# Optimization experiments

Measured on AMD Instinct MI355X. Metric: run time of the kernel, lower is better.

Reference implementation:

```python
import jax, jax.numpy as jnp
import numpy as np

N, E, ET, C, H, L = 100000, 500000, 3, 128, 128, 3
LN_EPS = 1e-5
L2_EPS = 1e-12


def setup_inputs() -> dict:
    ks = jax.random.split(jax.random.key(0), 12)
    s = 0.05
    return {
        "x": jax.random.normal(ks[0], (N, C), jnp.float32),
        "edges": jax.random.randint(ks[1], (ET, 2, E), 0, N),
        "Wp": jax.random.normal(ks[2], (ET, C, C), jnp.float32) * s,
        "bp": jax.random.normal(ks[3], (ET, C), jnp.float32) * s,
        "Wl0": jax.random.normal(ks[4], (ET, C, H), jnp.float32) * s,
        "bl0": jax.random.normal(ks[5], (ET, H), jnp.float32) * s,
        "Wr0": jax.random.normal(ks[6], (ET, C, H), jnp.float32) * s,
        "Wl": jax.random.normal(ks[7], (L - 1, ET, H, H), jnp.float32) * s,
        "bl": jax.random.normal(ks[8], (L - 1, ET, H), jnp.float32) * s,
        "Wr": jax.random.normal(ks[9], (L - 1, ET, H, H), jnp.float32) * s,
        "ln_g": jnp.ones((L - 1, H), jnp.float32),
        "ln_b": jnp.zeros((L - 1, H), jnp.float32),
    }


def _mean_aggr(msg, dst, n):
    # scatter-mean of per-edge messages onto destination nodes
    summed = jax.ops.segment_sum(msg, dst, num_segments=n)
    deg = jax.ops.segment_sum(jnp.ones((dst.shape[0],), msg.dtype), dst, num_segments=n)
    return summed / jnp.maximum(deg, 1.0)[:, None]


def _sage(h, ei, Wl_, bl_, Wr_, Wp_=None, bp_=None, normalize=False):
    # PyG SAGEConv: out = lin_l(mean_{j in N(i)} h_j) + lin_r(h_i)
    src, dst = ei[0], ei[1]
    hs = jax.nn.relu(h @ Wp_ + bp_) if Wp_ is not None else h  # project=True path
    agg = _mean_aggr(hs[src], dst, h.shape[0])
    out = agg @ Wl_ + bl_ + h @ Wr_
    if normalize:
        out = out / jnp.maximum(jnp.linalg.norm(out, axis=-1, keepdims=True), L2_EPS)
    return out


def _layer_norm(h, g, b):
    mu = h.mean(-1, keepdims=True)
    var = ((h - mu) ** 2).mean(-1, keepdims=True)
    return (h - mu) / jnp.sqrt(var + LN_EPS) * g + b


def _forward(x, edges, Wp, bp, Wl0, bl0, Wr0, Wl, bl, Wr, ln_g, ln_b):
    et = edges.shape[0]
    # layer 0: project=True, normalize=True; HeteroConv mean over edge types
    h = sum(_sage(x, edges[t], Wl0[t], bl0[t], Wr0[t], Wp[t], bp[t], True)
            for t in range(et)) / et
    h = _layer_norm(jax.nn.relu(h), ln_g[0], ln_b[0])  # dropout = identity (eval)
    n_rest = Wl.shape[0]
    for l in range(n_rest):
        h = sum(_sage(h, edges[t], Wl[l, t], bl[l, t], Wr[l, t])
                for t in range(et)) / et
        if l != n_rest - 1:
            h = _layer_norm(jax.nn.relu(h), ln_g[l + 1], ln_b[l + 1])
    return h


def reference(x, edges, Wp, bp, Wl0, bl0, Wr0, Wl, bl, Wr, ln_g, ln_b):
    return _forward(x, edges, Wp, bp, Wl0, bl0, Wr0, Wl, bl, Wr, ln_g, ln_b)
```

## Files before the change

### kernel.cpp

```cpp
#include <hip/hip_runtime.h>
#include <math.h>

#define CH 128
#define ETC 3
#define LN_EPS 1e-5f

typedef unsigned short u16;
typedef unsigned int u32;
typedef __attribute__((ext_vector_type(8))) short short8;
typedef __attribute__((ext_vector_type(4))) float f32x4;

__device__ __forceinline__ u16 f2bf(float f) {
    u32 u = __float_as_uint(f);
    u += 0x7FFFu + ((u >> 16) & 1u);
    return (u16)(u >> 16);
}
__device__ __forceinline__ float bflo(u32 u) { return __uint_as_float(u << 16); }
__device__ __forceinline__ float bfhi(u32 u) { return __uint_as_float(u & 0xFFFF0000u); }

__device__ __forceinline__ f32x4 mfma16(short8 a, short8 b, f32x4 c) {
    return __builtin_amdgcn_mfma_f32_16x16x32_bf16(a, b, c, 0, 0, 0);
}
__device__ __forceinline__ short8 ld8(const u16* p) { return *(const short8*)p; }

__global__ __launch_bounds__(256) void pack_w(
    const float* __restrict__ Wp, const float* __restrict__ Wl0,
    const float* __restrict__ Wr0, const float* __restrict__ Wl,
    const float* __restrict__ Wr, const float* __restrict__ bl,
    u16* __restrict__ Bswz, float* __restrict__ bls)
{
    if (blockIdx.x == 0) {
        int l = threadIdx.x >> 7, i = threadIdx.x & 127;
        bls[threadIdx.x] = (bl[((size_t)l * ETC + 0) * CH + i] +
                            bl[((size_t)l * ETC + 1) * CH + i] +
                            bl[((size_t)l * ETC + 2) * CH + i]) * (1.f / 3.f);
    }
    int grp = blockIdx.x * 256 + threadIdx.x;
    if (grp >= 17 * 2048) return;
    int lane = grp & 63;
    int t1 = grp >> 6;
    int nt = t1 & 7, t2 = t1 >> 3;
    int s = t2 & 3, mat = t2 >> 2;
    int q = lane >> 4, c = lane & 15;
    int nn = nt * 16 + c;

    const float* s0;
    const float* s1 = nullptr;
    const float* s2 = nullptr;
    float scale = 1.f;
    if (mat < 3) {
        s0 = Wp + (size_t)mat * CH * CH;
    } else if (mat < 9) {
        int t = (mat - 3) >> 1;
        s0 = ((mat - 3) & 1) ? Wr0 + (size_t)t * CH * CH : Wl0 + (size_t)t * CH * CH;
    } else {
        int l = (mat < 13) ? 0 : 1;
        int mm = mat - (l ? 13 : 9);
        scale = 1.f / 3.f;
        if (mm < 3) s0 = Wl + ((size_t)l * ETC + mm) * CH * CH;
        else {
            s0 = Wr + ((size_t)l * ETC + 0) * CH * CH;
            s1 = s0 + CH * CH;
            s2 = s1 + CH * CH;
        }
    }
    short8 o;
    #pragma unroll
    for (int j = 0; j < 8; ++j) {
        int k = s * 32 + q * 8 + j;
        float v = s0[(size_t)k * CH + nn];
        if (s1) v += s1[(size_t)k * CH + nn] + s2[(size_t)k * CH + nn];
        o[j] = (short)f2bf(v * scale);
    }
    *(short8*)&Bswz[(size_t)grp * 8] = o;
}

__global__ __launch_bounds__(256) void cast_x(
    const float* __restrict__ x, u16* __restrict__ xb, int total)
{
    int i = (blockIdx.x * 256 + threadIdx.x) * 8;
    if (i >= total) return;
    short8 o;
    #pragma unroll
    for (int j = 0; j < 8; ++j) o[j] = (short)f2bf(x[i + j]);
    *(short8*)&xb[i] = o;
}

template<int MODE, int RF>
__global__ __launch_bounds__(256, 2) void combine_k(
    const u16* __restrict__ agg0, const u16* __restrict__ agg1,
    const u16* __restrict__ agg2, const u16* __restrict__ self,
    const u16* __restrict__ Bs, const float* __restrict__ bias,
    const float* __restrict__ lg, const float* __restrict__ lb,
    u16* __restrict__ outb, float* __restrict__ outf, int nrows)
{
    __shared__ __align__(16) u16 Bsh[CH * CH];
    const int tid = threadIdx.x;
    const int w = tid >> 6, lane = tid & 63;
    const int q = lane >> 4, c = lane & 15;
    const int rbase = (blockIdx.x * 4 + w) * (RF * 16);
    const u16* aggs[3] = {agg0, agg1, agg2};
    constexpr int NM = (MODE == 0) ? 6 : ((MODE == 3) ? 1 : 4);

    f32x4 acc[RF][8] = {};
    f32x4 res[RF][8] = {};

    #pragma unroll
    for (int m = 0; m < NM; ++m) {
        __syncthreads();
        const u16* bsrc = Bs + (size_t)m * CH * CH;
        #pragma unroll
        for (int i = 0; i < 8; ++i)
            *(short8*)&Bsh[(i * 256 + tid) * 8] = ld8(&bsrc[(i * 256 + tid) * 8]);
        __syncthreads();

        const u16* A;
        if constexpr (MODE == 0)      A = (m & 1) ? self : aggs[m >> 1];
        else if constexpr (MODE == 3) A = self;
        else                          A = (m < 3) ? aggs[m] : self;

        #pragma unroll
        for (int s = 0; s < 4; ++s) {
            short8 af[RF];
            #pragma unroll
            for (int rf = 0; rf < RF; ++rf)
                af[rf] = ld8(&A[(size_t)(rbase + rf * 16 + c) * CH + s * 32 + q * 8]);
            #pragma unroll
            for (int nt = 0; nt < 8; ++nt) {
                short8 bv = *(const short8*)&Bsh[((size_t)(s * 8 + nt) * 64 + lane) * 8];
                #pragma unroll
                for (int rf = 0; rf < RF; ++rf)
                    acc[rf][nt] = mfma16(af[rf], bv, acc[rf][nt]);
            }
        }

        if constexpr (MODE == 0) {
            if (m & 1) {
                const int t = m >> 1;
                #pragma unroll
                for (int rf = 0; rf < RF; ++rf) {
                    float ss[4] = {0.f, 0.f, 0.f, 0.f};
                    #pragma unroll
                    for (int nt = 0; nt < 8; ++nt) {
                        float bf = bias[t * CH + nt * 16 + c];
                        #pragma unroll
                        for (int r = 0; r < 4; ++r) {
                            float v = acc[rf][nt][r] + bf;
                            acc[rf][nt][r] = v;
                            ss[r] += v * v;
                        }
                    }
                    #pragma unroll
                    for (int msk = 1; msk < 16; msk <<= 1)
                        #pragma unroll
                        for (int r = 0; r < 4; ++r) ss[r] += __shfl_xor(ss[r], msk, 64);
                    float sc[4];
                    #pragma unroll
                    for (int r = 0; r < 4; ++r)
                        sc[r] = 1.f / (3.f * fmaxf(sqrtf(ss[r]), 1e-12f));
                    #pragma unroll
                    for (int nt = 0; nt < 8; ++nt)
                        #pragma unroll
                        for (int r = 0; r < 4; ++r) {
                            res[rf][nt][r] += acc[rf][nt][r] * sc[r];
                            acc[rf][nt][r] = 0.f;
                        }
                }
            }
        }
    }

    if constexpr (MODE != 0) {
        #pragma unroll
        for (int nt = 0; nt < 8; ++nt) {
            float bv = bias[nt * 16 + c];
            #pragma unroll
            for (int rf = 0; rf < RF; ++rf)
                #pragma unroll
                for (int r = 0; r < 4; ++r) res[rf][nt][r] = acc[rf][nt][r] + bv;
        }
    }

    if constexpr (MODE == 2) {
        #pragma unroll
        for (int rf = 0; rf < RF; ++rf)
            #pragma unroll
            for (int nt = 0; nt < 8; ++nt)
                #pragma unroll
                for (int r = 0; r < 4; ++r) {
                    int row = rbase + rf * 16 + q * 4 + r;
                    if (row < nrows) outf[(size_t)row * CH + nt * 16 + c] = res[rf][nt][r];
                }
        return;
    }

    if constexpr (MODE == 3) {
        #pragma unroll
        for (int rf = 0; rf < RF; ++rf)
            #pragma unroll
            for (int nt = 0; nt < 8; ++nt)
                #pragma unroll
                for (int r = 0; r < 4; ++r) {
                    int row = rbase + rf * 16 + q * 4 + r;
                    outb[(size_t)row * CH + nt * 16 + c] = f2bf(fmaxf(res[rf][nt][r], 0.f));
                }
        return;
    }

    #pragma unroll
    for (int rf = 0; rf < RF; ++rf) {
        float s1[4] = {0.f, 0.f, 0.f, 0.f}, s2[4] = {0.f, 0.f, 0.f, 0.f};
        #pragma unroll
        for (int nt = 0; nt < 8; ++nt)
            #pragma unroll
            for (int r = 0; r < 4; ++r) {
                float v = fmaxf(res[rf][nt][r], 0.f);
                res[rf][nt][r] = v;
                s1[r] += v;
                s2[r] += v * v;
            }
        #pragma unroll
        for (int msk = 1; msk < 16; msk <<= 1)
            #pragma unroll
            for (int r = 0; r < 4; ++r) {
                s1[r] += __shfl_xor(s1[r], msk, 64);
                s2[r] += __shfl_xor(s2[r], msk, 64);
            }
        float mu[4], rs[4];
        #pragma unroll
        for (int r = 0; r < 4; ++r) {
            mu[r] = s1[r] * (1.f / 128.f);
            float var = s2[r] * (1.f / 128.f) - mu[r] * mu[r];
            rs[r] = rsqrtf(var + LN_EPS);
        }
        #pragma unroll
        for (int nt = 0; nt < 8; ++nt) {
            float gv = lg[nt * 16 + c], bv = lb[nt * 16 + c];
            #pragma unroll
            for (int r = 0; r < 4; ++r) {
                int row = rbase + rf * 16 + q * 4 + r;
                outb[(size_t)row * CH + nt * 16 + c] =
                    f2bf((res[rf][nt][r] - mu[r]) * rs[r] * gv + bv);
            }
        }
    }
}

__global__ __launch_bounds__(256) void agg_k(
    const u16* __restrict__ msg, const int* __restrict__ rowptr,
    const int* __restrict__ col, u16* __restrict__ agg, int n,
    int Ecap, unsigned long long aggstride)
{
    const int t = blockIdx.y;
    rowptr += (size_t)t * (n + 1);
    col += (size_t)t * Ecap;
    agg += (size_t)t * aggstride;

    int gid = blockIdx.x * 256 + threadIdx.x;
    int node = gid >> 5;
    int lane = threadIdx.x & 31;
    if (node >= n) return;
    int s = rowptr[node], e = rowptr[node + 1];
    const uint2* m64 = (const uint2*)msg;
    float a0 = 0.f, a1 = 0.f, a2 = 0.f, a3 = 0.f;
    float b0 = 0.f, b1 = 0.f, b2 = 0.f, b3 = 0.f;
    int j = s;
    for (; j + 2 <= e; j += 2) {
        int s0 = col[j], s1i = col[j + 1];
        uint2 v0 = m64[(size_t)s0 * 32 + lane];
        uint2 v1 = m64[(size_t)s1i * 32 + lane];
        a0 += bflo(v0.x); a1 += bfhi(v0.x); a2 += bflo(v0.y); a3 += bfhi(v0.y);
        b0 += bflo(v1.x); b1 += bfhi(v1.x); b2 += bflo(v1.y); b3 += bfhi(v1.y);
    }
    if (j < e) {
        int s0 = col[j];
        uint2 v0 = m64[(size_t)s0 * 32 + lane];
        a0 += bflo(v0.x); a1 += bfhi(v0.x); a2 += bflo(v0.y); a3 += bfhi(v0.y);
    }
    a0 += b0; a1 += b1; a2 += b2; a3 += b3;
    float inv = 1.f / (float)max(e - s, 1);
    uint2 o;
    o.x = (u32)f2bf(a0 * inv) | ((u32)f2bf(a1 * inv) << 16);
    o.y = (u32)f2bf(a2 * inv) | ((u32)f2bf(a3 * inv) << 16);
    ((uint2*)agg)[(size_t)node * 32 + lane] = o;
}

__global__ __launch_bounds__(256) void hist_k(
    const int* __restrict__ edges, int* __restrict__ cnt, int E, int n)
{
    int t = blockIdx.y;
    int e = blockIdx.x * 256 + threadIdx.x;
    if (e >= E) return;
    int dst = edges[(size_t)t * 2 * E + E + e];
    atomicAdd(&cnt[t * n + dst], 1);
}

__global__ __launch_bounds__(256) void scan1_k(
    const int* __restrict__ cnt, int* __restrict__ bsum, int n, int nbs)
{
    int t = blockIdx.y, b = blockIdx.x;
    int i = b * 256 + threadIdx.x;
    int v = (i < n) ? cnt[t * n + i] : 0;
    #pragma unroll
    for (int m = 1; m < 64; m <<= 1) v += __shfl_xor(v, m, 64);
    __shared__ int wsum[4];
    if ((threadIdx.x & 63) == 0) wsum[threadIdx.x >> 6] = v;
    __syncthreads();
    if (threadIdx.x == 0) bsum[t * nbs + b] = wsum[0] + wsum[1] + wsum[2] + wsum[3];
}

__global__ __launch_bounds__(512) void scan2_k(int* __restrict__ bsum, int nbs, int nb)
{
    int t = blockIdx.x;
    int tid = threadIdx.x;
    __shared__ int sh[512];
    int v = (tid < nb) ? bsum[t * nbs + tid] : 0;
    sh[tid] = v;
    __syncthreads();
    for (int off = 1; off < 512; off <<= 1) {
        int x = (tid >= off) ? sh[tid - off] : 0;
        __syncthreads();
        sh[tid] += x;
        __syncthreads();
    }
    if (tid < nb) bsum[t * nbs + tid] = sh[tid] - v;
}

__global__ __launch_bounds__(256) void scan3_k(
    const int* __restrict__ cnt, const int* __restrict__ bsum,
    int* __restrict__ rowptr, int n, int nbs)
{
    int t = blockIdx.y, b = blockIdx.x;
    int tid = threadIdx.x;
    int i = b * 256 + tid;
    __shared__ int sh[256];
    int v = (i < n) ? cnt[t * n + i] : 0;
    sh[tid] = v;
    __syncthreads();
    for (int off = 1; off < 256; off <<= 1) {
        int x = (tid >= off) ? sh[tid - off] : 0;
        __syncthreads();
        sh[tid] += x;
        __syncthreads();
    }
    int excl = sh[tid] - v + bsum[t * nbs + b];
    if (i < n) rowptr[(size_t)t * (n + 1) + i] = excl;
    if (i == n - 1) rowptr[(size_t)t * (n + 1) + n] = excl + v;
}

__global__ __launch_bounds__(256) void fill_k(
    const int* __restrict__ edges, const int* __restrict__ rowptr,
    int* __restrict__ cnt2, int* __restrict__ colbuf, int E, int n)
{
    int t = blockIdx.y;
    int e = blockIdx.x * 256 + threadIdx.x;
    if (e >= E) return;
    int src = edges[(size_t)t * 2 * E + e];
    int dst = edges[(size_t)t * 2 * E + E + e];
    int pos = rowptr[(size_t)t * (n + 1) + dst] + atomicAdd(&cnt2[t * n + dst], 1);
    colbuf[(size_t)t * E + pos] = src;
}

extern "C" void kernel_launch(void* const* d_in, const int* in_sizes, int n_in,
                              void* d_out, int out_size, void* d_ws, size_t ws_size,
                              hipStream_t stream) {
    const float* x    = (const float*)d_in[0];
    const int*   edges= (const int*)d_in[1];
    const float* Wp   = (const float*)d_in[2];
    const float* bp   = (const float*)d_in[3];
    const float* Wl0  = (const float*)d_in[4];
    const float* bl0  = (const float*)d_in[5];
    const float* Wr0  = (const float*)d_in[6];
    const float* Wl   = (const float*)d_in[7];
    const float* bl   = (const float*)d_in[8];
    const float* Wr   = (const float*)d_in[9];
    const float* ln_g = (const float*)d_in[10];
    const float* ln_b = (const float*)d_in[11];
    float* out = (float*)d_out;

    const int n  = in_sizes[0] / CH;
    const int E  = in_sizes[1] / (2 * ETC);
    const int npad = ((n + 255) / 256) * 256;
    const int NBS = 512;
    const int nb = (n + 255) / 256;
    const size_t MS = (size_t)CH * CH;

    char* p = (char*)d_ws;
    u16* xb   = (u16*)p;  p += (size_t)npad * CH * 2;
    u16* hs   = (u16*)p;  p += (size_t)npad * CH * 2;
    u16* agg  = (u16*)p;  p += (size_t)ETC * npad * CH * 2;
    u16* Bswz = (u16*)p;  p += 17 * MS * 2;
    float* bls = (float*)p; p += 256 * 4;
    int* cnt    = (int*)p;  p += (size_t)ETC * n * 4;
    int* rowptr = (int*)p;  p += (size_t)ETC * (n + 1) * 4;
    int* colbuf = (int*)p;  p += (size_t)ETC * E * 4;
    int* bsum   = (int*)p;

    const dim3 b256(256);
    const dim3 ge((E + 255) / 256, ETC);
    const dim3 gs(nb, ETC);
    const int gb2 = (n + 127) / 128;
    const int gb4 = (n + 255) / 256;
    const int ga = (n * 32 + 255) / 256;

    hipMemsetAsync(cnt, 0, (size_t)ETC * n * sizeof(int), stream);
    hist_k<<<ge, b256, 0, stream>>>(edges, cnt, E, n);
    scan1_k<<<gs, b256, 0, stream>>>(cnt, bsum, n, NBS);
    scan2_k<<<ETC, 512, 0, stream>>>(bsum, NBS, nb);
    scan3_k<<<gs, b256, 0, stream>>>(cnt, bsum, rowptr, n, NBS);
    hipMemsetAsync(cnt, 0, (size_t)ETC * n * sizeof(int), stream);
    fill_k<<<ge, b256, 0, stream>>>(edges, rowptr, cnt, colbuf, E, n);

    pack_w<<<136, b256, 0, stream>>>(Wp, Wl0, Wr0, Wl, Wr, bl, Bswz, bls);
    cast_x<<<(n * CH / 8 + 255) / 256, b256, 0, stream>>>(x, xb, n * CH);

    for (int t = 0; t < ETC; ++t) {
        combine_k<3, 4><<<gb4, b256, 0, stream>>>(
            nullptr, nullptr, nullptr, xb, Bswz + (size_t)t * MS, bp + t * CH,
            nullptr, nullptr, hs, nullptr, n);
        agg_k<<<dim3(ga, 1), b256, 0, stream>>>(hs, rowptr + (size_t)t * (n + 1),
                                                colbuf + (size_t)t * E,
                                                agg + (size_t)t * npad * CH, n, 0, 0ull);
    }
    combine_k<0, 2><<<gb2, b256, 0, stream>>>(agg, agg + (size_t)npad * CH,
                                              agg + (size_t)2 * npad * CH, xb,
                                              Bswz + 3 * MS, bl0, ln_g, ln_b, hs, nullptr, n);

    agg_k<<<dim3(ga, ETC), b256, 0, stream>>>(hs, rowptr, colbuf, agg, n, E,
                                              (unsigned long long)npad * CH);
    combine_k<1, 4><<<gb4, b256, 0, stream>>>(agg, agg + (size_t)npad * CH,
                                              agg + (size_t)2 * npad * CH, hs,
                                              Bswz + 9 * MS, bls, ln_g + CH, ln_b + CH,
                                              hs, nullptr, n);

    agg_k<<<dim3(ga, ETC), b256, 0, stream>>>(hs, rowptr, colbuf, agg, n, E,
                                              (unsigned long long)npad * CH);
    combine_k<2, 4><<<gb4, b256, 0, stream>>>(agg, agg + (size_t)npad * CH,
                                              agg + (size_t)2 * npad * CH, hs,
                                              Bswz + 13 * MS, bls + CH, nullptr, nullptr,
                                              nullptr, out, n);
}
```

Before: 690.5 us.

## Shrink combine tiles, drop res buffer outside mode 0, unroll gather by four

```diff
diff --git a/kernel.cpp b/kernel.cpp
--- a/kernel.cpp
+++ b/kernel.cpp
@@ -86,14 +86,15 @@
     *(short8*)&xb[i] = o;
 }
 
-template<int MODE, int RF>
-__global__ __launch_bounds__(256, 2) void combine_k(
+template<int MODE>
+__global__ __launch_bounds__(256) void combine_k(
     const u16* __restrict__ agg0, const u16* __restrict__ agg1,
     const u16* __restrict__ agg2, const u16* __restrict__ self,
     const u16* __restrict__ Bs, const float* __restrict__ bias,
     const float* __restrict__ lg, const float* __restrict__ lb,
     u16* __restrict__ outb, float* __restrict__ outf, int nrows)
 {
+    constexpr int RF = 2;
     __shared__ __align__(16) u16 Bsh[CH * CH];
     const int tid = threadIdx.x;
     const int w = tid >> 6, lane = tid & 63;
@@ -103,7 +104,13 @@
     constexpr int NM = (MODE == 0) ? 6 : ((MODE == 3) ? 1 : 4);
 
     f32x4 acc[RF][8] = {};
-    f32x4 res[RF][8] = {};
+    f32x4 res[RF][8];
+    if constexpr (MODE == 0) {
+        #pragma unroll
+        for (int rf = 0; rf < RF; ++rf)
+            #pragma unroll
+            for (int nt = 0; nt < 8; ++nt) res[rf][nt] = (f32x4){0.f, 0.f, 0.f, 0.f};
+    }
 
     #pragma unroll
     for (int m = 0; m < NM; ++m) {
@@ -177,7 +184,7 @@
             #pragma unroll
             for (int rf = 0; rf < RF; ++rf)
                 #pragma unroll
-                for (int r = 0; r < 4; ++r) res[rf][nt][r] = acc[rf][nt][r] + bv;
+                for (int r = 0; r < 4; ++r) acc[rf][nt][r] += bv;
         }
     }
 
@@ -189,7 +196,7 @@
                 #pragma unroll
                 for (int r = 0; r < 4; ++r) {
                     int row = rbase + rf * 16 + q * 4 + r;
-                    if (row < nrows) outf[(size_t)row * CH + nt * 16 + c] = res[rf][nt][r];
+                    if (row < nrows) outf[(size_t)row * CH + nt * 16 + c] = acc[rf][nt][r];
                 }
         return;
     }
@@ -202,11 +209,12 @@
                 #pragma unroll
                 for (int r = 0; r < 4; ++r) {
                     int row = rbase + rf * 16 + q * 4 + r;
-                    outb[(size_t)row * CH + nt * 16 + c] = f2bf(fmaxf(res[rf][nt][r], 0.f));
+                    outb[(size_t)row * CH + nt * 16 + c] = f2bf(fmaxf(acc[rf][nt][r], 0.f));
                 }
         return;
     }
 
+    auto& bank = (MODE == 0) ? res : acc;
     #pragma unroll
     for (int rf = 0; rf < RF; ++rf) {
         float s1[4] = {0.f, 0.f, 0.f, 0.f}, s2[4] = {0.f, 0.f, 0.f, 0.f};
@@ -214,8 +222,8 @@
         for (int nt = 0; nt < 8; ++nt)
             #pragma unroll
             for (int r = 0; r < 4; ++r) {
-                float v = fmaxf(res[rf][nt][r], 0.f);
-                res[rf][nt][r] = v;
+                float v = fmaxf(bank[rf][nt][r], 0.f);
+                bank[rf][nt][r] = v;
                 s1[r] += v;
                 s2[r] += v * v;
             }
@@ -240,7 +248,7 @@
             for (int r = 0; r < 4; ++r) {
                 int row = rbase + rf * 16 + q * 4 + r;
                 outb[(size_t)row * CH + nt * 16 + c] =
-                    f2bf((res[rf][nt][r] - mu[r]) * rs[r] * gv + bv);
+                    f2bf((bank[rf][nt][r] - mu[r]) * rs[r] * gv + bv);
             }
         }
     }
@@ -264,20 +272,26 @@
     const uint2* m64 = (const uint2*)msg;
     float a0 = 0.f, a1 = 0.f, a2 = 0.f, a3 = 0.f;
     float b0 = 0.f, b1 = 0.f, b2 = 0.f, b3 = 0.f;
+    float c0 = 0.f, c1 = 0.f, c2 = 0.f, c3 = 0.f;
+    float d0 = 0.f, d1 = 0.f, d2 = 0.f, d3 = 0.f;
     int j = s;
-    for (; j + 2 <= e; j += 2) {
-        int s0 = col[j], s1i = col[j + 1];
-        uint2 v0 = m64[(size_t)s0 * 32 + lane];
-        uint2 v1 = m64[(size_t)s1i * 32 + lane];
+    for (; j + 4 <= e; j += 4) {
+        int i0 = col[j], i1 = col[j + 1], i2 = col[j + 2], i3 = col[j + 3];
+        uint2 v0 = m64[(size_t)i0 * 32 + lane];
+        uint2 v1 = m64[(size_t)i1 * 32 + lane];
+        uint2 v2 = m64[(size_t)i2 * 32 + lane];
+        uint2 v3 = m64[(size_t)i3 * 32 + lane];
         a0 += bflo(v0.x); a1 += bfhi(v0.x); a2 += bflo(v0.y); a3 += bfhi(v0.y);
         b0 += bflo(v1.x); b1 += bfhi(v1.x); b2 += bflo(v1.y); b3 += bfhi(v1.y);
-    }
-    if (j < e) {
-        int s0 = col[j];
-        uint2 v0 = m64[(size_t)s0 * 32 + lane];
+        c0 += bflo(v2.x); c1 += bfhi(v2.x); c2 += bflo(v2.y); c3 += bfhi(v2.y);
+        d0 += bflo(v3.x); d1 += bfhi(v3.x); d2 += bflo(v3.y); d3 += bfhi(v3.y);
+    }
+    for (; j < e; ++j) {
+        int i0 = col[j];
+        uint2 v0 = m64[(size_t)i0 * 32 + lane];
         a0 += bflo(v0.x); a1 += bfhi(v0.x); a2 += bflo(v0.y); a3 += bfhi(v0.y);
     }
-    a0 += b0; a1 += b1; a2 += b2; a3 += b3;
+    a0 += b0 + c0 + d0; a1 += b1 + c1 + d1; a2 += b2 + c2 + d2; a3 += b3 + c3 + d3;
     float inv = 1.f / (float)max(e - s, 1);
     uint2 o;
     o.x = (u32)f2bf(a0 * inv) | ((u32)f2bf(a1 * inv) << 16);
@@ -380,7 +394,7 @@
 
     const int n  = in_sizes[0] / CH;
     const int E  = in_sizes[1] / (2 * ETC);
-    const int npad = ((n + 255) / 256) * 256;
+    const int npad = ((n + 127) / 128) * 128;
     const int NBS = 512;
     const int nb = (n + 255) / 256;
     const size_t MS = (size_t)CH * CH;
@@ -399,8 +413,7 @@
     const dim3 b256(256);
     const dim3 ge((E + 255) / 256, ETC);
     const dim3 gs(nb, ETC);
-    const int gb2 = (n + 127) / 128;
-    const int gb4 = (n + 255) / 256;
+    const int gb = (n + 127) / 128;
     const int ga = (n * 32 + 255) / 256;
 
     hipMemsetAsync(cnt, 0, (size_t)ETC * n * sizeof(int), stream);
@@ -415,28 +428,28 @@
     cast_x<<<(n * CH / 8 + 255) / 256, b256, 0, stream>>>(x, xb, n * CH);
 
     for (int t = 0; t < ETC; ++t) {
-        combine_k<3, 4><<<gb4, b256, 0, stream>>>(
+        combine_k<3><<<gb, b256, 0, stream>>>(
             nullptr, nullptr, nullptr, xb, Bswz + (size_t)t * MS, bp + t * CH,
             nullptr, nullptr, hs, nullptr, n);
         agg_k<<<dim3(ga, 1), b256, 0, stream>>>(hs, rowptr + (size_t)t * (n + 1),
                                                 colbuf + (size_t)t * E,
                                                 agg + (size_t)t * npad * CH, n, 0, 0ull);
     }
-    combine_k<0, 2><<<gb2, b256, 0, stream>>>(agg, agg + (size_t)npad * CH,
-                                              agg + (size_t)2 * npad * CH, xb,
-                                              Bswz + 3 * MS, bl0, ln_g, ln_b, hs, nullptr, n);
+    combine_k<0><<<gb, b256, 0, stream>>>(agg, agg + (size_t)npad * CH,
+                                          agg + (size_t)2 * npad * CH, xb,
+                                          Bswz + 3 * MS, bl0, ln_g, ln_b, hs, nullptr, n);
 
     agg_k<<<dim3(ga, ETC), b256, 0, stream>>>(hs, rowptr, colbuf, agg, n, E,
                                               (unsigned long long)npad * CH);
-    combine_k<1, 4><<<gb4, b256, 0, stream>>>(agg, agg + (size_t)npad * CH,
-                                              agg + (size_t)2 * npad * CH, hs,
-                                              Bswz + 9 * MS, bls, ln_g + CH, ln_b + CH,
-                                              hs, nullptr, n);
+    combine_k<1><<<gb, b256, 0, stream>>>(agg, agg + (size_t)npad * CH,
+                                          agg + (size_t)2 * npad * CH, hs,
+                                          Bswz + 9 * MS, bls, ln_g + CH, ln_b + CH,
+                                          hs, nullptr, n);
 
     agg_k<<<dim3(ga, ETC), b256, 0, stream>>>(hs, rowptr, colbuf, agg, n, E,
                                               (unsigned long long)npad * CH);
-    combine_k<2, 4><<<gb4, b256, 0, stream>>>(agg, agg + (size_t)npad * CH,
-                                              agg + (size_t)2 * npad * CH, hs,
-                                              Bswz + 13 * MS, bls + CH, nullptr, nullptr,
-                                              nullptr, out, n);
-}
+    combine_k<2><<<gb, b256, 0, stream>>>(agg, agg + (size_t)npad * CH,
+                                          agg + (size_t)2 * npad * CH, hs,
+                                          Bswz + 13 * MS, bls + CH, nullptr, nullptr,
+                                          nullptr, out, n);
+}
```

Result: slower. 706.2 us (+2.3%).
